# Kernel tuning notes

Measured on AMD Instinct MI355X. Metric: run time of the kernel, lower is better.

Reference implementation:

```python
import jax, jax.numpy as jnp
import numpy as np

D_MODEL, D_STATE, EXPAND = 1024, 32, 2
D_INNER = D_MODEL * EXPAND
B, L = 2, 2048


def setup_inputs() -> dict:
    key = jax.random.key(0)
    ks = jax.random.split(key, 10)
    s = 0.02
    return {
        "x": jax.random.normal(ks[0], (B, L, D_MODEL), dtype=jnp.float32),
        "W_in": jax.random.normal(ks[1], (D_INNER * 2, D_MODEL), dtype=jnp.float32) * s,
        "conv_w": jax.random.normal(ks[2], (D_INNER, 1, 3), dtype=jnp.float32) * 0.3,
        "conv_b": jax.random.normal(ks[3], (D_INNER,), dtype=jnp.float32) * 0.01,
        "A_log": jax.random.normal(ks[4], (D_INNER, D_STATE), dtype=jnp.float32),
        "D_skip": jnp.ones((D_INNER,), dtype=jnp.float32),
        "W_xproj": jax.random.normal(ks[5], (D_STATE * 2 + 1, D_INNER), dtype=jnp.float32) * s,
        "W_dt": jax.random.normal(ks[6], (D_INNER, 1), dtype=jnp.float32) * s,
        "b_dt": jax.random.normal(ks[7], (D_INNER,), dtype=jnp.float32) * 0.01,
        "alpha": jnp.asarray(0.5, dtype=jnp.float32),
        "W_out": jax.random.normal(ks[8], (D_MODEL, D_INNER), dtype=jnp.float32) * s,
    }


def _silu(v):
    return v * jax.nn.sigmoid(v)


def _forward(x, W_in, conv_w, conv_b, A_log, D_skip, W_xproj, W_dt, b_dt, alpha, W_out):
    # in_proj: (B, L, 2*d_inner) -> split into x_in, z
    xz = x @ W_in.T
    x_in, z = jnp.split(xz, 2, axis=-1)

    # depthwise conv1d, kernel 3, padding 1 (same-length, non-causal, as in source)
    xc = jax.lax.conv_general_dilated(
        x_in.transpose(0, 2, 1), conv_w, window_strides=(1,), padding=[(1, 1)],
        dimension_numbers=("NCH", "OIH", "NCH"), feature_group_count=D_INNER,
    ) + conv_b[None, :, None]
    x_conv = _silu(xc.transpose(0, 2, 1))  # (B, L, d_inner)

    # x_proj -> dt_raw (1), B_ssm (N), C_ssm (N)
    proj = x_conv @ W_xproj.T
    dt_raw = proj[..., :1]
    B_ssm = proj[..., 1:1 + D_STATE]
    C_ssm = proj[..., 1 + D_STATE:]
    dt = jax.nn.softplus(dt_raw @ W_dt.T + b_dt)  # (B, L, d_inner)

    A_real = -jnp.exp(A_log)           # (d_inner, d_state)
    a = jax.nn.sigmoid(alpha)

    def step(h, inp):
        dt_t, B_t, C_t, u_t = inp      # (B,d_inner), (B,N), (B,N), (B,d_inner)
        dtA = A_real[None] * dt_t[:, :, None]               # (B, d_inner, N)
        A_d = a * jnp.exp(dtA) + (1.0 - a) / (1.0 - 0.5 * dtA + 1e-6)
        h = A_d * h + (dt_t * u_t)[:, :, None] * B_t[:, None, :]
        y_t = jnp.einsum("bn,bdn->bd", C_t, h) + D_skip * u_t
        return h, y_t

    h0 = jnp.zeros((x.shape[0], D_INNER, D_STATE), dtype=x.dtype)
    xs = (dt.transpose(1, 0, 2), B_ssm.transpose(1, 0, 2),
          C_ssm.transpose(1, 0, 2), x_conv.transpose(1, 0, 2))
    _, ys = jax.lax.scan(step, h0, xs)   # (L, B, d_inner)
    y = ys.transpose(1, 0, 2) * _silu(z)
    return y @ W_out.T


def reference(x, W_in, conv_w, conv_b, A_log, D_skip, W_xproj, W_dt, b_dt, alpha, W_out):
    return _forward(x, W_in, conv_w, conv_b, A_log, D_skip, W_xproj, W_dt, b_dt, alpha, W_out)
```

## Files before the change

### kernel.cpp

```cpp
#include <hip/hip_runtime.h>

#define DM   1024
#define DI   2048
#define DST  32
#define NB   2
#define LSEQ 2048
#define BL   (NB*LSEQ)
#define LC   32
#define NC   64

using bf16   = __bf16;
using bf16x4 = __attribute__((ext_vector_type(4))) __bf16;
using bf16x8 = __attribute__((ext_vector_type(8))) __bf16;
using f32x4  = __attribute__((ext_vector_type(4))) float;
using f16x2  = __attribute__((ext_vector_type(2))) _Float16;

#define AS1(p) ((const __attribute__((address_space(1))) void*)(p))
#define AS3(p) ((__attribute__((address_space(3))) void*)(p))

static __device__ __forceinline__ float sigmoidf_(float x) {
  return 1.f / (1.f + __expf(-x));
}

static __device__ __forceinline__ f16x2 pack_f16x2(float a, float b) {
  return __builtin_bit_cast(f16x2, __builtin_amdgcn_cvt_pkrtz(a, b));
}

static __device__ __forceinline__ float exp2_(float x) {
#if __has_builtin(__builtin_amdgcn_exp2f)
  return __builtin_amdgcn_exp2f(x);
#else
  return exp2f(x);
#endif
}

__global__ __launch_bounds__(256) void cast_bf16_kernel(
    const float* __restrict__ in, bf16* __restrict__ out, int n4) {
  int i = blockIdx.x * 256 + threadIdx.x;
  if (i >= n4) return;
  f32x4 v = ((const f32x4*)in)[i];
  bf16x4 o;
  #pragma unroll
  for (int j = 0; j < 4; ++j) o[j] = (bf16)v[j];
  ((bf16x4*)out)[i] = o;
}

__global__ __launch_bounds__(256) void padcast_wxp_kernel(
    const float* __restrict__ in, bf16* __restrict__ out) {
  int i = blockIdx.x * 256 + threadIdx.x;
  int k4 = i & 511;
  int r  = i >> 9;
  int src = (r < 64) ? (r + 1) : ((r == 127) ? 0 : -1);
  f32x4 v = {0.f, 0.f, 0.f, 0.f};
  if (src >= 0) v = *(const f32x4*)(in + (size_t)src * 2048 + k4 * 4);
  bf16x4 o;
  #pragma unroll
  for (int j = 0; j < 4; ++j) o[j] = (bf16)v[j];
  ((bf16x4*)out)[i] = o;
}

__global__ __launch_bounds__(256) void gemm_lds(
    const bf16* __restrict__ A, const bf16* __restrict__ B,
    float* __restrict__ C, int M, int N, int K, int nz) {
  __shared__ bf16 As2[4][128][8];
  __shared__ bf16 Bs2[4][128][8];

  int tid  = threadIdx.x;
  int bm   = blockIdx.y, bn = blockIdx.x;
  int row0 = bm * 128, col0 = bn * 128;
  int w    = tid >> 6, lane = tid & 63;
  int wr   = w >> 1, wc = w & 1;
  int lr   = lane & 15, lk = lane >> 4;

  int seg = K / nz;
  int kb  = blockIdx.z * seg, ke = kb + seg;
  float* Cz = C + (size_t)blockIdx.z * ((size_t)M * N);

  f32x4 acc[4][4];
  #pragma unroll
  for (int i = 0; i < 4; ++i)
    #pragma unroll
    for (int j = 0; j < 4; ++j) acc[i][j] = f32x4{0.f, 0.f, 0.f, 0.f};

  int j0 = w * 64 + lane, j1 = 256 + w * 64 + lane;
  int ks0 = j0 >> 7, r0s = j0 & 127;
  int ks1 = j1 >> 7, r1s = j1 & 127;
  const bf16* Ag0 = A + (size_t)(row0 + r0s) * K + ks0 * 8;
  const bf16* Ag1 = A + (size_t)(row0 + r1s) * K + ks1 * 8;
  const bf16* Bg0 = B + (size_t)(col0 + r0s) * K + ks0 * 8;
  const bf16* Bg1 = B + (size_t)(col0 + r1s) * K + ks1 * 8;
  bf16* AsL = &As2[0][0][0];
  bf16* BsL = &Bs2[0][0][0];
  int base0 = (w * 64) * 8;
  int base1 = (256 + w * 64) * 8;

  for (int k0 = kb; k0 < ke; k0 += 32) {
    __builtin_amdgcn_global_load_lds(AS1(Ag0 + k0), AS3(AsL + base0), 16, 0, 0);
    __builtin_amdgcn_global_load_lds(AS1(Ag1 + k0), AS3(AsL + base1), 16, 0, 0);
    __builtin_amdgcn_global_load_lds(AS1(Bg0 + k0), AS3(BsL + base0), 16, 0, 0);
    __builtin_amdgcn_global_load_lds(AS1(Bg1 + k0), AS3(BsL + base1), 16, 0, 0);
    __syncthreads();

    bf16x8 af[4], bff[4];
    #pragma unroll
    for (int mi = 0; mi < 4; ++mi)
      af[mi] = *(const bf16x8*)&As2[lk][wr * 64 + mi * 16 + lr][0];
    #pragma unroll
    for (int ni = 0; ni < 4; ++ni)
      bff[ni] = *(const bf16x8*)&Bs2[lk][wc * 64 + ni * 16 + lr][0];

    #pragma unroll
    for (int mi = 0; mi < 4; ++mi)
      #pragma unroll
      for (int ni = 0; ni < 4; ++ni)
        acc[mi][ni] = __builtin_amdgcn_mfma_f32_16x16x32_bf16(
            af[mi], bff[ni], acc[mi][ni], 0, 0, 0);
    __syncthreads();
  }

  #pragma unroll
  for (int mi = 0; mi < 4; ++mi)
    #pragma unroll
    for (int ni = 0; ni < 4; ++ni) {
      int r0 = row0 + wr * 64 + mi * 16 + lk * 4;
      int c  = col0 + wc * 64 + ni * 16 + lr;
      #pragma unroll
      for (int r = 0; r < 4; ++r)
        Cz[(size_t)(r0 + r) * N + c] = acc[mi][ni][r];
    }
}

__global__ __launch_bounds__(256) void reduce_proj_kernel(
    const float* __restrict__ part, float* __restrict__ proj) {
  int i = blockIdx.x * 256 + threadIdx.x;
  f32x4 s = ((const f32x4*)part)[i];
  #pragma unroll
  for (int z = 1; z < 8; ++z) s += ((const f32x4*)part)[(size_t)z * 131072 + i];
  ((f32x4*)proj)[i] = s;
}

__global__ __launch_bounds__(256) void conv_silu_kernel(
    const float* __restrict__ xz, bf16* __restrict__ xconv,
    const float* __restrict__ conv_w, const float* __restrict__ conv_b) {
  int i = blockIdx.x * 256 + threadIdx.x;
  int d4 = i & 511;
  int d  = d4 * 4;
  int bl = i >> 9;
  int l  = bl & (LSEQ - 1);

  const float* base = xz + (size_t)bl * (2 * DI) + d;
  f32x4 zero = {0.f, 0.f, 0.f, 0.f};
  f32x4 xm = (l > 0)        ? *(const f32x4*)(base - 2 * DI) : zero;
  f32x4 xc = *(const f32x4*)(base);
  f32x4 xp = (l < LSEQ - 1) ? *(const f32x4*)(base + 2 * DI) : zero;

  bf16x4 o;
  #pragma unroll
  for (int j = 0; j < 4; ++j) {
    float w0 = conv_w[(d + j) * 3 + 0];
    float w1 = conv_w[(d + j) * 3 + 1];
    float w2 = conv_w[(d + j) * 3 + 2];
    float v = fmaf(w0, xm[j], fmaf(w1, xc[j], fmaf(w2, xp[j], conv_b[d + j])));
    v = v * sigmoidf_(v);
    o[j] = (bf16)v;
  }
  *(bf16x4*)(xconv + (size_t)bl * DI + d) = o;
}

__global__ __launch_bounds__(256) void dtprep_kernel(
    const float* __restrict__ proj, const bf16* __restrict__ xconv,
    const float* __restrict__ W_dt, const float* __restrict__ b_dt,
    unsigned int* __restrict__ dtp) {
  int i = blockIdx.x * 256 + threadIdx.x;
  int d4 = (i & 511) * 4;
  int bl = i >> 9;
  float dtraw = proj[(size_t)bl * 128 + 127];
  f32x4 wd = *(const f32x4*)(W_dt + d4);
  f32x4 bd = *(const f32x4*)(b_dt + d4);
  bf16x4 uu = *(const bf16x4*)(xconv + (size_t)bl * DI + d4);
  uint4 o;
  #pragma unroll
  for (int j = 0; j < 4; ++j) {
    float s  = fmaf(dtraw, wd[j], bd[j]);
    float dt = (s > 15.f) ? s : __logf(1.f + __expf(s));
    float dtu = dt * (float)uu[j];
    f16x2 pk = pack_f16x2(dt, dtu);
    ((unsigned int*)&o)[j] = __builtin_bit_cast(unsigned int, pk);
  }
  *(uint4*)(dtp + (size_t)bl * 4096 + d4) = o;
}


__global__ __launch_bounds__(256, 6) void scan_phase1(
    const float* __restrict__ proj, const unsigned int* __restrict__ dtp,
    const float* __restrict__ A_log, const float* __restrict__ alpha,
    unsigned int* __restrict__ PH) {
  __shared__ float Bs[LC][32];
  int tid = threadIdx.x;
  int wid = tid >> 6, lane = tid & 63;
  int dl = lane & 31, nh = lane >> 5;
  int d = blockIdx.x * 128 + wid * 32 + dl;
  int b = blockIdx.y, c = blockIdx.z;
  int n0 = nh * 16;

  const float* pb = proj + ((size_t)b * LSEQ + c * LC) * 128;

  {
    const float* g = pb + (size_t)(tid >> 3) * 128 + (tid & 7) * 4;
    __builtin_amdgcn_global_load_lds(AS1(g), AS3((char*)&Bs[0][0] + wid * 1024),
                                     16, 0, 0);
  }

  float aG = sigmoidf_(alpha[0]), omA = 1.f - aG;

  float Ar2[16];
  #pragma unroll
  for (int n = 0; n < 16; n += 4) {
    f32x4 al = *(const f32x4*)(A_log + (size_t)d * DST + n0 + n);
    #pragma unroll
    for (int j = 0; j < 4; ++j) Ar2[n + j] = -__expf(al[j]) * 1.44269504f;
  }

  const unsigned int* dc = dtp + ((size_t)b * LSEQ + c * LC) * 4096 + d;

  float h[16], P[16];
  #pragma unroll
  for (int n = 0; n < 16; ++n) { h[n] = 0.f; P[n] = 1.f; }

  __syncthreads();

  unsigned int dwn = dc[0];
  #pragma unroll 2
  for (int t = 0; t < LC; ++t) {
    f16x2 dw = __builtin_bit_cast(f16x2, dwn);
    dwn = dc[(size_t)(t + 1) * 4096];
    float dt = (float)dw[0], dtu = (float)dw[1];
    #pragma unroll
    for (int n4 = 0; n4 < 4; ++n4) {
      f32x4 Bq = *(const f32x4*)&Bs[t][((n0 + n4 * 4) & 31)];
      #pragma unroll
      for (int j = 0; j < 4; ++j) {
        int n = n4 * 4 + j;
        float t1  = dt * Ar2[n];
        float ex  = exp2_(t1);
        float den = fmaf(t1, -0.34657359f, 1.000001f);
        float Ad  = fmaf(aG, ex, omA * __builtin_amdgcn_rcpf(den));
        P[n] *= Ad;
        h[n] = fmaf(Ad, h[n], dtu * Bq[j]);
      }
    }
  }
  size_t ob = (((size_t)c * NB + b) * DI + d) * DST + n0;
  #pragma unroll
  for (int n4 = 0; n4 < 4; ++n4) {
    uint4 o;
    #pragma unroll
    for (int j = 0; j < 4; ++j) {
      int n = n4 * 4 + j;
      ((unsigned int*)&o)[j] =
          __builtin_bit_cast(unsigned int, pack_f16x2(P[n], h[n]));
    }
    *(uint4*)(PH + ob + n4 * 4) = o;
  }
}

__global__ __launch_bounds__(256) void scan_phase2(unsigned int* __restrict__ PH) {
  int i = blockIdx.x * 256 + threadIdx.x;
  float H = 0.f;
  #pragma unroll 4
  for (int c = 0; c < NC; ++c) {
    size_t idx = (size_t)c * (NB * DI * DST) + i;
    f16x2 ph = __builtin_bit_cast(f16x2, PH[idx]);
    ((float*)PH)[idx] = H;
    H = fmaf((float)ph[0], H, (float)ph[1]);
  }
}

__global__ __launch_bounds__(256, 6) void scan_phase3(
    const float* __restrict__ proj, const unsigned int* __restrict__ dtp,
    const float* __restrict__ xzf,
    const bf16* __restrict__ xconv,
    const float* __restrict__ A_log, const float* __restrict__ D_skip,
    const float* __restrict__ alpha, const float* __restrict__ PH,
    bf16* __restrict__ yb) {
  __shared__ float BCs[LC][64];
  int tid = threadIdx.x;
  int wid = tid >> 6, lane = tid & 63;
  int dl = lane & 31, nh = lane >> 5;
  int d = blockIdx.x * 128 + wid * 32 + dl;
  int b = blockIdx.y, c = blockIdx.z;
  int n0 = nh * 16;

  const float* pb = proj + ((size_t)b * LSEQ + c * LC) * 128;

  {
    const float* g0 = pb + (size_t)(tid >> 4) * 128 + (tid & 15) * 4;
    int s1 = tid + 256;
    const float* g1 = pb + (size_t)(s1 >> 4) * 128 + (s1 & 15) * 4;
    char* base = (char*)&BCs[0][0];
    __builtin_amdgcn_global_load_lds(AS1(g0), AS3(base + wid * 1024), 16, 0, 0);
    __builtin_amdgcn_global_load_lds(AS1(g1), AS3(base + 4096 + wid * 1024),
                                     16, 0, 0);
  }

  float aG = sigmoidf_(alpha[0]), omA = 1.f - aG;
  float Dsk = D_skip[d];

  float Ar2[16];
  #pragma unroll
  for (int n = 0; n < 16; n += 4) {
    f32x4 al = *(const f32x4*)(A_log + (size_t)d * DST + n0 + n);
    #pragma unroll
    for (int j = 0; j < 4; ++j) Ar2[n + j] = -__expf(al[j]) * 1.44269504f;
  }

  float h[16];
  size_t ob = (((size_t)c * NB + b) * DI + d) * DST + n0;
  #pragma unroll
  for (int n = 0; n < 16; n += 4) {
    f32x4 hv = *(const f32x4*)((const float*)PH + ob + n);
    #pragma unroll
    for (int j = 0; j < 4; ++j) h[n + j] = hv[j];
  }

  const unsigned int* dc = dtp + ((size_t)b * LSEQ + c * LC) * 4096 + d;
  const bf16*  uc = xconv + ((size_t)b * LSEQ + c * LC) * DI + d;
  const float* zc = xzf + ((size_t)b * LSEQ + c * LC) * 4096 + 2048 + d;
  bf16*        yc = yb  + ((size_t)b * LSEQ + c * LC) * DI + d;

  __syncthreads();

  unsigned int dwn = dc[0];
  #pragma unroll 2
  for (int t = 0; t < LC; ++t) {
    f16x2 dw = __builtin_bit_cast(f16x2, dwn);
    dwn = dc[(size_t)(t + 1) * 4096];
    float dt = (float)dw[0], dtu = (float)dw[1];
    float p0 = 0.f, p1 = 0.f, p2 = 0.f, p3 = 0.f;
    #pragma unroll
    for (int n4 = 0; n4 < 4; ++n4) {
      f32x4 Bq = *(const f32x4*)&BCs[t][n0 + n4 * 4];
      f32x4 Cq = *(const f32x4*)&BCs[t][32 + n0 + n4 * 4];
      #pragma unroll
      for (int j = 0; j < 4; ++j) {
        int n = n4 * 4 + j;
        float t1  = dt * Ar2[n];
        float ex  = exp2_(t1);
        float den = fmaf(t1, -0.34657359f, 1.000001f);
        float Ad  = fmaf(aG, ex, omA * __builtin_amdgcn_rcpf(den));
        h[n] = fmaf(Ad, h[n], dtu * Bq[j]);
        if (j == 0)      p0 = fmaf(Cq[j], h[n], p0);
        else if (j == 1) p1 = fmaf(Cq[j], h[n], p1);
        else if (j == 2) p2 = fmaf(Cq[j], h[n], p2);
        else             p3 = fmaf(Cq[j], h[n], p3);
      }
    }
    float part = (p0 + p1) + (p2 + p3);
    part += __shfl_xor(part, 32);
    if (nh == 0) {
      float u = (float)uc[(size_t)t * DI];
      float z = zc[(size_t)t * 4096];
      float y = fmaf(Dsk, u, part);
      y *= z * sigmoidf_(z);
      yc[(size_t)t * DI] = (bf16)y;
    }
  }
}

extern "C" void kernel_launch(void* const* d_in, const int* in_sizes, int n_in,
                              void* d_out, int out_size, void* d_ws, size_t ws_size,
                              hipStream_t stream) {
  const float* x      = (const float*)d_in[0];
  const float* W_in   = (const float*)d_in[1];
  const float* conv_w = (const float*)d_in[2];
  const float* conv_b = (const float*)d_in[3];
  const float* A_log  = (const float*)d_in[4];
  const float* D_skip = (const float*)d_in[5];
  const float* W_xprj = (const float*)d_in[6];
  const float* W_dt   = (const float*)d_in[7];
  const float* b_dt   = (const float*)d_in[8];
  const float* alpha  = (const float*)d_in[9];
  const float* W_out  = (const float*)d_in[10];

  char* ws = (char*)d_ws;
  float* xz    = (float*)(ws + 0);
  bf16*  xconv = (bf16*) (ws + 67108864);
  float* proj  = (float*)(ws + 83886080);
  bf16*  woutb = (bf16*) (ws + 85983232);
  bf16*  wxpb  = (bf16*) (ws + 90177536);
  bf16*  yb    = (bf16*) (ws + 90701824);
  unsigned int* PH = (unsigned int*)(ws + 107479040);
  bf16*  xb    = (bf16*) (ws + 107479040);
  bf16*  winb  = (bf16*) (ws + 115867648);
  float* projp = (float*)(ws + 107479040);
  unsigned int* dtp = (unsigned int*)xz;

  float* out = (float*)d_out;

  cast_bf16_kernel<<<4096, 256, 0, stream>>>(x, xb, BL * DM / 4);
  cast_bf16_kernel<<<4096, 256, 0, stream>>>(W_in, winb, 2 * DI * DM / 4);
  cast_bf16_kernel<<<2048, 256, 0, stream>>>(W_out, woutb, DM * DI / 4);
  padcast_wxp_kernel<<<256, 256, 0, stream>>>(W_xprj, wxpb);

  gemm_lds<<<dim3(32, 32, 1), 256, 0, stream>>>(xb, winb, xz, BL, 2 * DI, DM, 1);

  conv_silu_kernel<<<8192, 256, 0, stream>>>(xz, xconv, conv_w, conv_b);

  gemm_lds<<<dim3(1, 32, 8), 256, 0, stream>>>(xconv, wxpb, projp, BL, 128, DI, 8);
  reduce_proj_kernel<<<512, 256, 0, stream>>>(projp, proj);

  dtprep_kernel<<<8192, 256, 0, stream>>>(proj, xconv, W_dt, b_dt, dtp);

  scan_phase1<<<dim3(DI / 128, NB, NC), 256, 0, stream>>>(proj, dtp, A_log,
                                                          alpha, PH);
  scan_phase2<<<512, 256, 0, stream>>>(PH);
  scan_phase3<<<dim3(DI / 128, NB, NC), 256, 0, stream>>>(proj, dtp, xz, xconv,
                                                          A_log, D_skip, alpha,
                                                          (const float*)PH, yb);

  gemm_lds<<<dim3(8, 32, 1), 256, 0, stream>>>(yb, woutb, out, BL, DM, DI, 1);
}
```

Before: 396.1 us.

## Fuse dt softplus prep into scan phases and split-K the output GEMM

The separate dtprep kernel, which wrote packed dt and dt*u values to a workspace buffer, is removed. Both scan phases now stage dt_raw for the chunk in shared memory and compute the softplus and dt*u inline, reading u directly from xconv. This drops one launch and a full-size intermediate write and read, at the cost of redundant transcendental work per thread. Separately, the final output GEMM is split over K into two partial buffers and summed by a new reduce kernel, raising block count at the cost of extra partial-output traffic.

```diff
diff --git a/kernel.cpp b/kernel.cpp
--- a/kernel.cpp
+++ b/kernel.cpp
@@ -139,6 +139,14 @@
   ((f32x4*)proj)[i] = s;
 }
 
+__global__ __launch_bounds__(256) void reduce_out_kernel(
+    const float* __restrict__ part, float* __restrict__ out) {
+  int i = blockIdx.x * 256 + threadIdx.x;
+  f32x4 s = ((const f32x4*)part)[i];
+  s += ((const f32x4*)part)[(size_t)1048576 + i];
+  ((f32x4*)out)[i] = s;
+}
+
 __global__ __launch_bounds__(256) void conv_silu_kernel(
     const float* __restrict__ xz, bf16* __restrict__ xconv,
     const float* __restrict__ conv_w, const float* __restrict__ conv_b) {
@@ -167,35 +175,14 @@
   *(bf16x4*)(xconv + (size_t)bl * DI + d) = o;
 }
 
-__global__ __launch_bounds__(256) void dtprep_kernel(
+
+__global__ __launch_bounds__(256, 6) void scan_phase1(
     const float* __restrict__ proj, const bf16* __restrict__ xconv,
-    const float* __restrict__ W_dt, const float* __restrict__ b_dt,
-    unsigned int* __restrict__ dtp) {
-  int i = blockIdx.x * 256 + threadIdx.x;
-  int d4 = (i & 511) * 4;
-  int bl = i >> 9;
-  float dtraw = proj[(size_t)bl * 128 + 127];
-  f32x4 wd = *(const f32x4*)(W_dt + d4);
-  f32x4 bd = *(const f32x4*)(b_dt + d4);
-  bf16x4 uu = *(const bf16x4*)(xconv + (size_t)bl * DI + d4);
-  uint4 o;
-  #pragma unroll
-  for (int j = 0; j < 4; ++j) {
-    float s  = fmaf(dtraw, wd[j], bd[j]);
-    float dt = (s > 15.f) ? s : __logf(1.f + __expf(s));
-    float dtu = dt * (float)uu[j];
-    f16x2 pk = pack_f16x2(dt, dtu);
-    ((unsigned int*)&o)[j] = __builtin_bit_cast(unsigned int, pk);
-  }
-  *(uint4*)(dtp + (size_t)bl * 4096 + d4) = o;
-}
-
-
-__global__ __launch_bounds__(256, 6) void scan_phase1(
-    const float* __restrict__ proj, const unsigned int* __restrict__ dtp,
-    const float* __restrict__ A_log, const float* __restrict__ alpha,
+    const float* __restrict__ A_log, const float* __restrict__ W_dt,
+    const float* __restrict__ b_dt, const float* __restrict__ alpha,
     unsigned int* __restrict__ PH) {
   __shared__ float Bs[LC][32];
+  __shared__ float Ds[LC];
   int tid = threadIdx.x;
   int wid = tid >> 6, lane = tid & 63;
   int dl = lane & 31, nh = lane >> 5;
@@ -210,8 +197,10 @@
     __builtin_amdgcn_global_load_lds(AS1(g), AS3((char*)&Bs[0][0] + wid * 1024),
                                      16, 0, 0);
   }
+  if (tid < LC) Ds[tid] = pb[(size_t)tid * 128 + 127];
 
   float aG = sigmoidf_(alpha[0]), omA = 1.f - aG;
+  float Wd = W_dt[d], bd = b_dt[d];
 
   float Ar2[16];
   #pragma unroll
@@ -221,7 +210,7 @@
     for (int j = 0; j < 4; ++j) Ar2[n + j] = -__expf(al[j]) * 1.44269504f;
   }
 
-  const unsigned int* dc = dtp + ((size_t)b * LSEQ + c * LC) * 4096 + d;
+  const bf16* uc = xconv + ((size_t)b * LSEQ + c * LC) * DI + d;
 
   float h[16], P[16];
   #pragma unroll
@@ -229,12 +218,13 @@
 
   __syncthreads();
 
-  unsigned int dwn = dc[0];
-  #pragma unroll 2
+  #pragma unroll 4
   for (int t = 0; t < LC; ++t) {
-    f16x2 dw = __builtin_bit_cast(f16x2, dwn);
-    dwn = dc[(size_t)(t + 1) * 4096];
-    float dt = (float)dw[0], dtu = (float)dw[1];
+    float dtraw = Ds[t];
+    float u = (float)uc[(size_t)t * DI];
+    float s = fmaf(dtraw, Wd, bd);
+    float dt = (s > 15.f) ? s : __logf(1.f + __expf(s));
+    float dtu = dt * u;
     #pragma unroll
     for (int n4 = 0; n4 < 4; ++n4) {
       f32x4 Bq = *(const f32x4*)&Bs[t][((n0 + n4 * 4) & 31)];
@@ -277,13 +267,14 @@
 }
 
 __global__ __launch_bounds__(256, 6) void scan_phase3(
-    const float* __restrict__ proj, const unsigned int* __restrict__ dtp,
+    const float* __restrict__ proj, const bf16* __restrict__ xconv,
     const float* __restrict__ xzf,
-    const bf16* __restrict__ xconv,
     const float* __restrict__ A_log, const float* __restrict__ D_skip,
+    const float* __restrict__ W_dt, const float* __restrict__ b_dt,
     const float* __restrict__ alpha, const float* __restrict__ PH,
     bf16* __restrict__ yb) {
   __shared__ float BCs[LC][64];
+  __shared__ float Ds[LC];
   int tid = threadIdx.x;
   int wid = tid >> 6, lane = tid & 63;
   int dl = lane & 31, nh = lane >> 5;
@@ -302,9 +293,11 @@
     __builtin_amdgcn_global_load_lds(AS1(g1), AS3(base + 4096 + wid * 1024),
                                      16, 0, 0);
   }
+  if (tid < LC) Ds[tid] = pb[(size_t)tid * 128 + 127];
 
   float aG = sigmoidf_(alpha[0]), omA = 1.f - aG;
   float Dsk = D_skip[d];
+  float Wd = W_dt[d], bd = b_dt[d];
 
   float Ar2[16];
   #pragma unroll
@@ -318,24 +311,24 @@
   size_t ob = (((size_t)c * NB + b) * DI + d) * DST + n0;
   #pragma unroll
   for (int n = 0; n < 16; n += 4) {
-    f32x4 hv = *(const f32x4*)((const float*)PH + ob + n);
+    f32x4 hv = *(const f32x4*)(PH + ob + n);
     #pragma unroll
     for (int j = 0; j < 4; ++j) h[n + j] = hv[j];
   }
 
-  const unsigned int* dc = dtp + ((size_t)b * LSEQ + c * LC) * 4096 + d;
   const bf16*  uc = xconv + ((size_t)b * LSEQ + c * LC) * DI + d;
   const float* zc = xzf + ((size_t)b * LSEQ + c * LC) * 4096 + 2048 + d;
   bf16*        yc = yb  + ((size_t)b * LSEQ + c * LC) * DI + d;
 
   __syncthreads();
 
-  unsigned int dwn = dc[0];
-  #pragma unroll 2
+  #pragma unroll 4
   for (int t = 0; t < LC; ++t) {
-    f16x2 dw = __builtin_bit_cast(f16x2, dwn);
-    dwn = dc[(size_t)(t + 1) * 4096];
-    float dt = (float)dw[0], dtu = (float)dw[1];
+    float dtraw = Ds[t];
+    float u = (float)uc[(size_t)t * DI];
+    float s = fmaf(dtraw, Wd, bd);
+    float dt = (s > 15.f) ? s : __logf(1.f + __expf(s));
+    float dtu = dt * u;
     float p0 = 0.f, p1 = 0.f, p2 = 0.f, p3 = 0.f;
     #pragma unroll
     for (int n4 = 0; n4 < 4; ++n4) {
@@ -358,7 +351,6 @@
     float part = (p0 + p1) + (p2 + p3);
     part += __shfl_xor(part, 32);
     if (nh == 0) {
-      float u = (float)uc[(size_t)t * DI];
       float z = zc[(size_t)t * 4096];
       float y = fmaf(Dsk, u, part);
       y *= z * sigmoidf_(z);
@@ -393,7 +385,7 @@
   bf16*  xb    = (bf16*) (ws + 107479040);
   bf16*  winb  = (bf16*) (ws + 115867648);
   float* projp = (float*)(ws + 107479040);
-  unsigned int* dtp = (unsigned int*)xz;
+  float* outp  = (float*)(ws + 107479040);
 
   float* out = (float*)d_out;
 
@@ -409,14 +401,14 @@
   gemm_lds<<<dim3(1, 32, 8), 256, 0, stream>>>(xconv, wxpb, projp, BL, 128, DI, 8);
   reduce_proj_kernel<<<512, 256, 0, stream>>>(projp, proj);
 
-  dtprep_kernel<<<8192, 256, 0, stream>>>(proj, xconv, W_dt, b_dt, dtp);
-
-  scan_phase1<<<dim3(DI / 128, NB, NC), 256, 0, stream>>>(proj, dtp, A_log,
-                                                          alpha, PH);
+  scan_phase1<<<dim3(DI / 128, NB, NC), 256, 0, stream>>>(proj, xconv, A_log,
+                                                          W_dt, b_dt, alpha, PH);
   scan_phase2<<<512, 256, 0, stream>>>(PH);
-  scan_phase3<<<dim3(DI / 128, NB, NC), 256, 0, stream>>>(proj, dtp, xz, xconv,
-                                                          A_log, D_skip, alpha,
+  scan_phase3<<<dim3(DI / 128, NB, NC), 256, 0, stream>>>(proj, xconv, xz,
+                                                          A_log, D_skip, W_dt,
+                                                          b_dt, alpha,
                                                           (const float*)PH, yb);
 
-  gemm_lds<<<dim3(8, 32, 1), 256, 0, stream>>>(yb, woutb, out, BL, DM, DI, 1);
-}
+  gemm_lds<<<dim3(8, 32, 2), 256, 0, stream>>>(yb, woutb, outp, BL, DM, DI, 2);
+  reduce_out_kernel<<<4096, 256, 0, stream>>>(outp, out);
+}
```

Measured after the change: 465.9 us. 17.6% more time.
